# Kernel tuning notes

Hardware: AMD Instinct MI355X
Metric: run time of the kernel (lower is better)

The kernel has to match this reference:

```python
import jax, jax.numpy as jnp
import numpy as np

B, T, D, H = 64, 2048, 256, 256


def setup_inputs() -> dict:
    key = jax.random.key(0)
    ks = jax.random.split(key, 8)
    s = 1.0 / np.sqrt(H)
    return {
        "inputs": jax.random.normal(ks[0], (B, T, D), dtype=jnp.float32),
        "hidden_state": jax.random.normal(ks[1], (2, B, H), dtype=jnp.float32),
        "W_ih_f": jax.random.normal(ks[2], (H, D), dtype=jnp.float32) * s,
        "W_hh_f": jax.random.normal(ks[3], (H, H), dtype=jnp.float32) * s,
        "b_f": jax.random.normal(ks[4], (H,), dtype=jnp.float32) * s,
        "W_ih_r": jax.random.normal(ks[5], (H, D), dtype=jnp.float32) * s,
        "W_hh_r": jax.random.normal(ks[6], (H, H), dtype=jnp.float32) * s,
        "b_r": jax.random.normal(ks[7], (H,), dtype=jnp.float32) * s,
    }


def _run_dir(xs_tm, h0, W_ih, W_hh, b, reverse):
    # xs_tm: [T, B, D] time-major; h0: [B, H]
    # Precompute the input projection for all timesteps in one GEMM.
    x_proj = jnp.einsum('tbd,hd->tbh', xs_tm, W_ih) + b  # [T, B, H]

    def step(h, xp):
        h_new = jnp.tanh(xp + h @ W_hh.T)  # [B, H]
        return h_new, h_new

    h_last, outs = jax.lax.scan(step, h0, x_proj, reverse=reverse)
    return outs, h_last  # outs: [T, B, H] in original time order


def reference(inputs, hidden_state, W_ih_f, W_hh_f, b_f, W_ih_r, W_hh_r, b_r):
    xs_tm = jnp.transpose(inputs, (1, 0, 2))  # [T, B, D]
    out_f, h_f = _run_dir(xs_tm, hidden_state[0], W_ih_f, W_hh_f, b_f, reverse=False)
    out_r, h_r = _run_dir(xs_tm, hidden_state[1], W_ih_r, W_hh_r, b_r, reverse=True)
    outputs = jnp.concatenate([out_f, out_r], axis=-1)  # [T, B, 2H]
    outputs = jnp.transpose(outputs, (1, 0, 2))  # [B, T, 2H]
    out_hidden = jnp.stack([h_f, h_r], axis=0)  # [2, B, H]
    return outputs, out_hidden
```

## Files before the change

kernel.cpp:

```cpp
#include <hip/hip_runtime.h>
#include <hip/hip_bf16.h>

#define T_LEN 2048
#define BATCH 64
#define DIM   256
#define HID   256

using f16    = _Float16;
using f16x8  = __attribute__((ext_vector_type(8))) _Float16;
using fp16x2 = __attribute__((ext_vector_type(2))) __fp16;
using f32x4  = __attribute__((ext_vector_type(4))) float;

__device__ __forceinline__ f16x8 pack8(float4 a, float4 b)
{
    fp16x2 p0 = __builtin_amdgcn_cvt_pkrtz(a.x, a.y);
    fp16x2 p1 = __builtin_amdgcn_cvt_pkrtz(a.z, a.w);
    fp16x2 p2 = __builtin_amdgcn_cvt_pkrtz(b.x, b.y);
    fp16x2 p3 = __builtin_amdgcn_cvt_pkrtz(b.z, b.w);
    f16x8 r = { (f16)p0.x, (f16)p0.y, (f16)p1.x, (f16)p1.y,
                (f16)p2.x, (f16)p2.y, (f16)p3.x, (f16)p3.y };
    return r;
}

__global__ __launch_bounds__(256) void xproj_gemm(
    const float* __restrict__ x, const float* __restrict__ Wf,
    const float* __restrict__ Wr, const float* __restrict__ bf,
    const float* __restrict__ br, float* __restrict__ out)
{
    __shared__ __align__(16) f16 As[128 * 64];
    __shared__ __align__(16) f16 Bs[128 * 64];

    const int tid = threadIdx.x;
    const long m0 = (long)blockIdx.x * 128;
    const int  n0 = blockIdx.y * 128;
    const float* Bsrc = (n0 < 256) ? (Wf + (long)n0 * DIM)
                                   : (Wr + (long)(n0 - 256) * DIM);
    const int w = tid >> 6, l = tid & 63;
    const int wm = (w & 1) * 64, wn = (w >> 1) * 64;
    const int srow = tid >> 1, sseg = tid & 1;

    f32x4 acc[4][4] = {};

    for (int kk = 0; kk < DIM; kk += 64) {
        __syncthreads();
        {
            const float* sa = x + (m0 + srow) * DIM + kk + sseg * 32;
            #pragma unroll
            for (int q = 0; q < 4; ++q) {
                float4 u0 = ((const float4*)sa)[q * 2];
                float4 u1 = ((const float4*)sa)[q * 2 + 1];
                int c = (sseg * 4 + q) ^ (srow & 7);
                *(f16x8*)(&As[srow * 64 + c * 8]) = pack8(u0, u1);
            }
        }
        {
            const float* sb = Bsrc + (long)srow * DIM + kk + sseg * 32;
            #pragma unroll
            for (int q = 0; q < 4; ++q) {
                float4 u0 = ((const float4*)sb)[q * 2];
                float4 u1 = ((const float4*)sb)[q * 2 + 1];
                int c = (sseg * 4 + q) ^ (srow & 7);
                *(f16x8*)(&Bs[srow * 64 + c * 8]) = pack8(u0, u1);
            }
        }
        __syncthreads();

        #pragma unroll
        for (int kt = 0; kt < 2; ++kt) {
            f16x8 a[4], b[4];
            #pragma unroll
            for (int im = 0; im < 4; ++im) {
                int row = wm + im * 16 + (l & 15);
                int c   = (kt * 4 + (l >> 4)) ^ (row & 7);
                a[im] = *(const f16x8*)(&As[row * 64 + c * 8]);
            }
            #pragma unroll
            for (int in = 0; in < 4; ++in) {
                int row = wn + in * 16 + (l & 15);
                int c   = (kt * 4 + (l >> 4)) ^ (row & 7);
                b[in] = *(const f16x8*)(&Bs[row * 64 + c * 8]);
            }
            #pragma unroll
            for (int im = 0; im < 4; ++im)
                #pragma unroll
                for (int in = 0; in < 4; ++in)
                    acc[im][in] = __builtin_amdgcn_mfma_f32_16x16x32_f16(
                        a[im], b[in], acc[im][in], 0, 0, 0);
        }
    }

    #pragma unroll
    for (int im = 0; im < 4; ++im)
        #pragma unroll
        for (int in = 0; in < 4; ++in) {
            int n = n0 + wn + in * 16 + (l & 15);
            float bias = (n < 256) ? bf[n] : br[n - 256];
            #pragma unroll
            for (int r = 0; r < 4; ++r) {
                long m = m0 + wm + im * 16 + ((l >> 4) * 4 + r);
                out[m * 512 + n] = acc[im][in][r] + bias;
            }
        }
}

__global__ __launch_bounds__(256, 1) void rnn_scan(
    float* __restrict__ out, const float* __restrict__ hidden,
    const float* __restrict__ Whf, const float* __restrict__ Whr,
    float* __restrict__ hid_out)
{
    __shared__ __align__(16) f16 hbuf[2][16 * 256];

    const int tid = threadIdx.x;
    const int g   = blockIdx.x;
    const int dir = g >> 2;
    const int b0  = (g & 3) * 16;
    const int w   = tid >> 6, l = tid & 63;
    const int c15 = l & 15, hi = l >> 4;

    const float* Wh = dir ? Whr : Whf;
    f16x8 Bhh[4][8];
    #pragma unroll
    for (int nt = 0; nt < 4; ++nt) {
        int n = w * 64 + nt * 16 + c15;
        #pragma unroll
        for (int kt = 0; kt < 8; ++kt) {
            const float* p = Wh + (long)n * HID + kt * 32 + hi * 8;
            float4 u0 = ((const float4*)p)[0];
            float4 u1 = ((const float4*)p)[1];
            f16x8 r = { (f16)u0.x, (f16)u0.y, (f16)u0.z, (f16)u0.w,
                        (f16)u1.x, (f16)u1.y, (f16)u1.z, (f16)u1.w };
            Bhh[nt][kt] = r;
        }
    }

    {
        int chain = tid >> 4;
        int cbase = (tid & 15) * 16;
        const float* hp = hidden + ((long)dir * BATCH + b0 + chain) * HID + cbase;
        #pragma unroll
        for (int cc = 0; cc < 2; ++cc) {
            float4 u0 = ((const float4*)hp)[cc * 2];
            float4 u1 = ((const float4*)hp)[cc * 2 + 1];
            f16x8 r = { (f16)u0.x, (f16)u0.y, (f16)u0.z, (f16)u0.w,
                        (f16)u1.x, (f16)u1.y, (f16)u1.z, (f16)u1.w };
            int c  = (cbase >> 3) + cc;
            int cs = c ^ (chain & 7);
            *(f16x8*)(&hbuf[0][chain * 256 + cs * 8]) = r;
        }
    }

    unsigned off[4][4];
    float    xr[4][4];
    const int t0 = dir ? (T_LEN - 1) : 0;
    #pragma unroll
    for (int nt = 0; nt < 4; ++nt)
        #pragma unroll
        for (int r = 0; r < 4; ++r) {
            int chain = hi * 4 + r;
            int col   = w * 64 + nt * 16 + c15;
            off[nt][r] = (unsigned)((((b0 + chain) * T_LEN + t0) * 512
                                     + dir * 256 + col) * 4);
            xr[nt][r] = *(const float*)((const char*)out + off[nt][r]);
        }

    __syncthreads();

    const int sdelta = dir ? -2048 : 2048;
    float hlast[4][4];

    for (int s = 0; s < T_LEN; ++s) {
        const f16* rb = hbuf[s & 1];
        f16*       wb = hbuf[(s + 1) & 1];
        const int d = (s == T_LEN - 1) ? 0 : sdelta;

        f32x4 acc[4];
        #pragma unroll
        for (int nt = 0; nt < 4; ++nt)
            #pragma unroll
            for (int r = 0; r < 4; ++r)
                acc[nt][r] = xr[nt][r];

        #pragma unroll
        for (int nt = 0; nt < 4; ++nt)
            #pragma unroll
            for (int r = 0; r < 4; ++r) {
                off[nt][r] += d;
                xr[nt][r] = *(const float*)((const char*)out + off[nt][r]);
            }

        f16x8 hfrag[8];
        #pragma unroll
        for (int kt = 0; kt < 8; ++kt) {
            int cs = ((kt * 4 + hi) ^ (c15 & 7));
            hfrag[kt] = *(const f16x8*)(&rb[c15 * 256 + cs * 8]);
        }

        #pragma unroll
        for (int kt = 0; kt < 8; ++kt)
            #pragma unroll
            for (int nt = 0; nt < 4; ++nt)
                acc[nt] = __builtin_amdgcn_mfma_f32_16x16x32_f16(
                    hfrag[kt], Bhh[nt][kt], acc[nt], 0, 0, 0);

        #pragma unroll
        for (int nt = 0; nt < 4; ++nt)
            #pragma unroll
            for (int r = 0; r < 4; ++r) {
                float p  = acc[nt][r];
                float e  = __builtin_amdgcn_exp2f(p * 2.885390081777927f);
                float hn = fmaf(-2.0f, __builtin_amdgcn_rcpf(e + 1.0f), 1.0f);
                hlast[nt][r] = hn;
                *(float*)((char*)out + (off[nt][r] - d)) = hn;

                int chain = hi * 4 + r;
                int col   = w * 64 + nt * 16 + c15;
                int cs    = (col >> 3) ^ (chain & 7);
                wb[chain * 256 + cs * 8 + (col & 7)] = (f16)hn;
            }

        asm volatile("s_waitcnt lgkmcnt(0)" ::: "memory");
        __builtin_amdgcn_sched_barrier(0);
        __builtin_amdgcn_s_barrier();
        __builtin_amdgcn_sched_barrier(0);
    }

    #pragma unroll
    for (int nt = 0; nt < 4; ++nt)
        #pragma unroll
        for (int r = 0; r < 4; ++r) {
            int chain = hi * 4 + r;
            int col   = w * 64 + nt * 16 + c15;
            hid_out[((long)dir * BATCH + b0 + chain) * HID + col] = hlast[nt][r];
        }
}

extern "C" void kernel_launch(void* const* d_in, const int* in_sizes, int n_in,
                              void* d_out, int out_size, void* d_ws, size_t ws_size,
                              hipStream_t stream)
{
    const float* x      = (const float*)d_in[0];
    const float* hidden = (const float*)d_in[1];
    const float* W_ih_f = (const float*)d_in[2];
    const float* W_hh_f = (const float*)d_in[3];
    const float* b_f    = (const float*)d_in[4];
    const float* W_ih_r = (const float*)d_in[5];
    const float* W_hh_r = (const float*)d_in[6];
    const float* b_r    = (const float*)d_in[7];

    float* outp    = (float*)d_out;
    float* hid_out = outp + (long)BATCH * T_LEN * 512;

    xproj_gemm<<<dim3((BATCH * T_LEN) / 128, 512 / 128), 256, 0, stream>>>(
        x, W_ih_f, W_ih_r, b_f, b_r, outp);

    rnn_scan<<<dim3(8), 256, 0, stream>>>(
        outp, hidden, W_hh_f, W_hh_r, hid_out);
}
```

Baseline: 2.498 ms.

## Double-buffer projection GEMM with XCD-aware block mapping; split scan over 8 waves

The input-projection GEMM now uses double-buffered shared memory with register prefetch of the next K-slice, and a 1D grid whose block index is remapped so neighbouring tiles land on the same XCD. The recurrent scan kernel moves from 4 to 8 waves per block, with each wave owning 32 hidden columns instead of 64. This halves the per-wave MFMA chain on the serial critical path of each timestep. In exchange the block-wide barrier now synchronises 8 waves, and shared-memory use in the GEMM doubles.

```diff
diff --git a/kernel.cpp b/kernel.cpp
--- a/kernel.cpp
+++ b/kernel.cpp
@@ -22,49 +22,53 @@
     return r;
 }
 
-__global__ __launch_bounds__(256) void xproj_gemm(
+__global__ __launch_bounds__(256, 2) void xproj_gemm(
     const float* __restrict__ x, const float* __restrict__ Wf,
     const float* __restrict__ Wr, const float* __restrict__ bf,
     const float* __restrict__ br, float* __restrict__ out)
 {
-    __shared__ __align__(16) f16 As[128 * 64];
-    __shared__ __align__(16) f16 Bs[128 * 64];
+    __shared__ __align__(16) f16 As[2][128 * 64];
+    __shared__ __align__(16) f16 Bs[2][128 * 64];
 
     const int tid = threadIdx.x;
-    const long m0 = (long)blockIdx.x * 128;
-    const int  n0 = blockIdx.y * 128;
+    const int id  = blockIdx.x;
+    const int xcd = id & 7;
+    const int g   = id >> 3;
+    const int bx  = xcd * 128 + (g >> 2);
+    const int by  = g & 3;
+
+    const long m0 = (long)bx * 128;
+    const int  n0 = by * 128;
     const float* Bsrc = (n0 < 256) ? (Wf + (long)n0 * DIM)
                                    : (Wr + (long)(n0 - 256) * DIM);
     const int w = tid >> 6, l = tid & 63;
     const int wm = (w & 1) * 64, wn = (w >> 1) * 64;
     const int srow = tid >> 1, sseg = tid & 1;
 
+    const float* sa_base = x + (m0 + srow) * DIM + sseg * 32;
+    const float* sb_base = Bsrc + (long)srow * DIM + sseg * 32;
+
+    float4 Ra[8], Rb[8];
+
+    auto LD = [&](int kk) {
+        #pragma unroll
+        for (int q = 0; q < 8; ++q) {
+            Ra[q] = ((const float4*)(sa_base + kk))[q];
+            Rb[q] = ((const float4*)(sb_base + kk))[q];
+        }
+    };
+    auto ST = [&](int buf) {
+        #pragma unroll
+        for (int q = 0; q < 4; ++q) {
+            int c = (sseg * 4 + q) ^ (srow & 7);
+            *(f16x8*)(&As[buf][srow * 64 + c * 8]) = pack8(Ra[2*q], Ra[2*q+1]);
+            *(f16x8*)(&Bs[buf][srow * 64 + c * 8]) = pack8(Rb[2*q], Rb[2*q+1]);
+        }
+    };
+
     f32x4 acc[4][4] = {};
 
-    for (int kk = 0; kk < DIM; kk += 64) {
-        __syncthreads();
-        {
-            const float* sa = x + (m0 + srow) * DIM + kk + sseg * 32;
-            #pragma unroll
-            for (int q = 0; q < 4; ++q) {
-                float4 u0 = ((const float4*)sa)[q * 2];
-                float4 u1 = ((const float4*)sa)[q * 2 + 1];
-                int c = (sseg * 4 + q) ^ (srow & 7);
-                *(f16x8*)(&As[srow * 64 + c * 8]) = pack8(u0, u1);
-            }
-        }
-        {
-            const float* sb = Bsrc + (long)srow * DIM + kk + sseg * 32;
-            #pragma unroll
-            for (int q = 0; q < 4; ++q) {
-                float4 u0 = ((const float4*)sb)[q * 2];
-                float4 u1 = ((const float4*)sb)[q * 2 + 1];
-                int c = (sseg * 4 + q) ^ (srow & 7);
-                *(f16x8*)(&Bs[srow * 64 + c * 8]) = pack8(u0, u1);
-            }
-        }
-        __syncthreads();
-
+    auto COMPUTE = [&](int buf) {
         #pragma unroll
         for (int kt = 0; kt < 2; ++kt) {
             f16x8 a[4], b[4];
@@ -72,13 +76,13 @@
             for (int im = 0; im < 4; ++im) {
                 int row = wm + im * 16 + (l & 15);
                 int c   = (kt * 4 + (l >> 4)) ^ (row & 7);
-                a[im] = *(const f16x8*)(&As[row * 64 + c * 8]);
+                a[im] = *(const f16x8*)(&As[buf][row * 64 + c * 8]);
             }
             #pragma unroll
             for (int in = 0; in < 4; ++in) {
                 int row = wn + in * 16 + (l & 15);
                 int c   = (kt * 4 + (l >> 4)) ^ (row & 7);
-                b[in] = *(const f16x8*)(&Bs[row * 64 + c * 8]);
+                b[in] = *(const f16x8*)(&Bs[buf][row * 64 + c * 8]);
             }
             #pragma unroll
             for (int im = 0; im < 4; ++im)
@@ -87,7 +91,19 @@
                     acc[im][in] = __builtin_amdgcn_mfma_f32_16x16x32_f16(
                         a[im], b[in], acc[im][in], 0, 0, 0);
         }
-    }
+    };
+
+    LD(0);
+    ST(0);
+    __syncthreads();
+    #pragma unroll
+    for (int k = 0; k < 3; ++k) {
+        LD((k + 1) * 64);
+        COMPUTE(k & 1);
+        ST((k + 1) & 1);
+        __syncthreads();
+    }
+    COMPUTE(1);
 
     #pragma unroll
     for (int im = 0; im < 4; ++im)
@@ -103,7 +119,7 @@
         }
 }
 
-__global__ __launch_bounds__(256, 1) void rnn_scan(
+__global__ __launch_bounds__(512, 2) void rnn_scan(
     float* __restrict__ out, const float* __restrict__ hidden,
     const float* __restrict__ Whf, const float* __restrict__ Whr,
     float* __restrict__ hid_out)
@@ -118,10 +134,10 @@
     const int c15 = l & 15, hi = l >> 4;
 
     const float* Wh = dir ? Whr : Whf;
-    f16x8 Bhh[4][8];
-    #pragma unroll
-    for (int nt = 0; nt < 4; ++nt) {
-        int n = w * 64 + nt * 16 + c15;
+    f16x8 Bhh[2][8];
+    #pragma unroll
+    for (int nt = 0; nt < 2; ++nt) {
+        int n = w * 32 + nt * 16 + c15;
         #pragma unroll
         for (int kt = 0; kt < 8; ++kt) {
             const float* p = Wh + (long)n * HID + kt * 32 + hi * 8;
@@ -134,30 +150,26 @@
     }
 
     {
-        int chain = tid >> 4;
-        int cbase = (tid & 15) * 16;
-        const float* hp = hidden + ((long)dir * BATCH + b0 + chain) * HID + cbase;
-        #pragma unroll
-        for (int cc = 0; cc < 2; ++cc) {
-            float4 u0 = ((const float4*)hp)[cc * 2];
-            float4 u1 = ((const float4*)hp)[cc * 2 + 1];
-            f16x8 r = { (f16)u0.x, (f16)u0.y, (f16)u0.z, (f16)u0.w,
-                        (f16)u1.x, (f16)u1.y, (f16)u1.z, (f16)u1.w };
-            int c  = (cbase >> 3) + cc;
-            int cs = c ^ (chain & 7);
-            *(f16x8*)(&hbuf[0][chain * 256 + cs * 8]) = r;
-        }
-    }
-
-    unsigned off[4][4];
-    float    xr[4][4];
+        int chain = tid >> 5;
+        int c     = tid & 31;
+        const float* hp = hidden + ((long)dir * BATCH + b0 + chain) * HID + c * 8;
+        float4 u0 = ((const float4*)hp)[0];
+        float4 u1 = ((const float4*)hp)[1];
+        f16x8 r = { (f16)u0.x, (f16)u0.y, (f16)u0.z, (f16)u0.w,
+                    (f16)u1.x, (f16)u1.y, (f16)u1.z, (f16)u1.w };
+        int cs = c ^ (chain & 7);
+        *(f16x8*)(&hbuf[0][chain * 256 + cs * 8]) = r;
+    }
+
+    unsigned off[2][4];
+    float    xr[2][4];
     const int t0 = dir ? (T_LEN - 1) : 0;
     #pragma unroll
-    for (int nt = 0; nt < 4; ++nt)
+    for (int nt = 0; nt < 2; ++nt)
         #pragma unroll
         for (int r = 0; r < 4; ++r) {
             int chain = hi * 4 + r;
-            int col   = w * 64 + nt * 16 + c15;
+            int col   = w * 32 + nt * 16 + c15;
             off[nt][r] = (unsigned)((((b0 + chain) * T_LEN + t0) * 512
                                      + dir * 256 + col) * 4);
             xr[nt][r] = *(const float*)((const char*)out + off[nt][r]);
@@ -166,22 +178,22 @@
     __syncthreads();
 
     const int sdelta = dir ? -2048 : 2048;
-    float hlast[4][4];
+    float hlast[2][4];
 
     for (int s = 0; s < T_LEN; ++s) {
         const f16* rb = hbuf[s & 1];
         f16*       wb = hbuf[(s + 1) & 1];
         const int d = (s == T_LEN - 1) ? 0 : sdelta;
 
-        f32x4 acc[4];
-        #pragma unroll
-        for (int nt = 0; nt < 4; ++nt)
+        f32x4 acc[2];
+        #pragma unroll
+        for (int nt = 0; nt < 2; ++nt)
             #pragma unroll
             for (int r = 0; r < 4; ++r)
                 acc[nt][r] = xr[nt][r];
 
         #pragma unroll
-        for (int nt = 0; nt < 4; ++nt)
+        for (int nt = 0; nt < 2; ++nt)
             #pragma unroll
             for (int r = 0; r < 4; ++r) {
                 off[nt][r] += d;
@@ -198,12 +210,12 @@
         #pragma unroll
         for (int kt = 0; kt < 8; ++kt)
             #pragma unroll
-            for (int nt = 0; nt < 4; ++nt)
+            for (int nt = 0; nt < 2; ++nt)
                 acc[nt] = __builtin_amdgcn_mfma_f32_16x16x32_f16(
                     hfrag[kt], Bhh[nt][kt], acc[nt], 0, 0, 0);
 
         #pragma unroll
-        for (int nt = 0; nt < 4; ++nt)
+        for (int nt = 0; nt < 2; ++nt)
             #pragma unroll
             for (int r = 0; r < 4; ++r) {
                 float p  = acc[nt][r];
@@ -213,7 +225,7 @@
                 *(float*)((char*)out + (off[nt][r] - d)) = hn;
 
                 int chain = hi * 4 + r;
-                int col   = w * 64 + nt * 16 + c15;
+                int col   = w * 32 + nt * 16 + c15;
                 int cs    = (col >> 3) ^ (chain & 7);
                 wb[chain * 256 + cs * 8 + (col & 7)] = (f16)hn;
             }
@@ -225,11 +237,11 @@
     }
 
     #pragma unroll
-    for (int nt = 0; nt < 4; ++nt)
+    for (int nt = 0; nt < 2; ++nt)
         #pragma unroll
         for (int r = 0; r < 4; ++r) {
             int chain = hi * 4 + r;
-            int col   = w * 64 + nt * 16 + c15;
+            int col   = w * 32 + nt * 16 + c15;
             hid_out[((long)dir * BATCH + b0 + chain) * HID + col] = hlast[nt][r];
         }
 }
@@ -250,9 +262,9 @@
     float* outp    = (float*)d_out;
     float* hid_out = outp + (long)BATCH * T_LEN * 512;
 
-    xproj_gemm<<<dim3((BATCH * T_LEN) / 128, 512 / 128), 256, 0, stream>>>(
+    xproj_gemm<<<dim3(4096), 256, 0, stream>>>(
         x, W_ih_f, W_ih_r, b_f, b_r, outp);
 
-    rnn_scan<<<dim3(8), 256, 0, stream>>>(
+    rnn_scan<<<dim3(8), 512, 0, stream>>>(
         outp, hidden, W_hh_f, W_hh_r, hid_out);
 }
```

After: 2.529 ms. Within noise of the previous version (+1.2%).
